# Performance work log

Measured on AMD Instinct MI355X. Metric: run time of the kernel, lower is better.

The kernel has to match this reference:

```python
import jax, jax.numpy as jnp
import numpy as np

SPARSITY = 0.1  # fraction of entries kept (set to 1)


def _subnet(scores, k):
    # Mirrors GetSubnet.forward: full sort of flattened |scores|, zero the
    # lowest j = int((1-k)*n) ranks, set the rest to 1 (ties broken by sort order).
    flat = scores.ravel()
    n = flat.size
    j = int((1.0 - k) * n)  # static python int
    order = jnp.argsort(flat)  # ascending
    out = jnp.zeros((n,), dtype=scores.dtype).at[order[j:]].set(1)
    return out.reshape(scores.shape)


def setup_inputs() -> dict:
    key = jax.random.key(0)
    kA, kB = jax.random.split(key)
    # kaiming_uniform_(a=sqrt(5)) => U(-bound, bound), bound = sqrt(6/((1+5)*fan_in)) = 1/sqrt(fan_in)
    A_shape = (1024, 16384)
    B_shape = (16384, 1024)
    bA = 1.0 / np.sqrt(A_shape[1])
    bB = 1.0 / np.sqrt(B_shape[1])
    lora_A_mask = jax.random.uniform(kA, A_shape, jnp.float32, -bA, bA)
    lora_B_mask = jax.random.uniform(kB, B_shape, jnp.float32, -bB, bB)
    return {"lora_A_mask": lora_A_mask, "lora_B_mask": lora_B_mask}


def reference(lora_A_mask, lora_B_mask):
    mask_A = _subnet(jnp.abs(lora_A_mask), SPARSITY)
    mask_B = _subnet(jnp.abs(lora_B_mask), SPARSITY)
    return (mask_A, mask_B)
```

## Files before the change

### kernel.cpp

```cpp
#include <hip/hip_runtime.h>
#include <stdint.h>

#define OFF_H1     0u
#define OFF_H2     2048u
#define OFF_H3     4096u
#define OFF_PREFIX 6144u
#define OFF_RANK   6145u
#define OFF_T      6146u
#define OFF_C      6147u
#define OFF_CNT    6148u
#define OFF_BCNT   6656u
#define OFF_BUF    7168u
#define CAP        8192u
#define MAT_WORDS  (7168u + 2u * CAP)
#define SUB        4
#define NB2        512
#define SEGCAP     16384u

__global__ void init_k(uint32_t* __restrict__ ws) {
  uint32_t i = blockIdx.x * blockDim.x + threadIdx.x;
  if (i < 6656u) { ws[i] = 0u; ws[MAT_WORDS + i] = 0u; }
}

__global__ void hist1_k(const float* __restrict__ A, const float* __restrict__ B,
                        uint32_t* __restrict__ ws, int nvec) {
  const int m = blockIdx.y;
  const float4* __restrict__ src = (const float4*)(m == 0 ? A : B);
  uint32_t* W = ws + (size_t)m * MAT_WORDS;
  __shared__ uint32_t h[2048 * SUB];
  for (int i = threadIdx.x; i < 2048 * SUB; i += blockDim.x) h[i] = 0u;
  __syncthreads();
  const uint32_t sub = threadIdx.x & (SUB - 1);
  int idx0 = blockIdx.x * blockDim.x + threadIdx.x;
  int stride = gridDim.x * blockDim.x;
  for (int i = idx0; i < nvec; i += stride) {
    float4 f = src[i];
    const float v[4] = {f.x, f.y, f.z, f.w};
#pragma unroll
    for (int c = 0; c < 4; c++) {
      uint32_t u = __float_as_uint(v[c]) & 0x7fffffffu;
      atomicAdd(&h[(u >> 21) * SUB + sub], 1u);
    }
  }
  __syncthreads();
  uint32_t* gh = W + OFF_H1;
  for (int b = threadIdx.x; b < 2048; b += blockDim.x) {
    uint32_t s = 0u;
#pragma unroll
    for (int k = 0; k < SUB; k++) s += h[b * SUB + k];
    if (s) atomicAdd(&gh[b], s);
  }
}

__global__ void hist2_k(const float* __restrict__ A, const float* __restrict__ B,
                        uint32_t* __restrict__ ws, uint32_t* __restrict__ outbuf,
                        int nvec) {
  const int m = blockIdx.y;
  const float4* __restrict__ src = (const float4*)(m == 0 ? A : B);
  uint32_t* W = ws + (size_t)m * MAT_WORDS;
  uint32_t* seg = outbuf + (size_t)m * 16777216u + (size_t)blockIdx.x * (SEGCAP * 2u);
  __shared__ uint32_t h[2048 * SUB];
  __shared__ uint32_t segn;
  for (int i = threadIdx.x; i < 2048 * SUB; i += blockDim.x) h[i] = 0u;
  if (threadIdx.x == 0) segn = 0u;
  uint32_t prefix = W[OFF_PREFIX];
  __syncthreads();
  const uint32_t sub = threadIdx.x & (SUB - 1);
  int idx0 = blockIdx.x * blockDim.x + threadIdx.x;
  int stride = gridDim.x * blockDim.x;
  for (int i = idx0; i < nvec; i += stride) {
    float4 f = src[i];
    const float v[4] = {f.x, f.y, f.z, f.w};
#pragma unroll
    for (int c = 0; c < 4; c++) {
      uint32_t u = __float_as_uint(v[c]) & 0x7fffffffu;
      if ((u >> 21) == (prefix >> 21)) {
        atomicAdd(&h[((u >> 10) & 2047u) * SUB + sub], 1u);
        uint32_t s = atomicAdd(&segn, 1u);
        if (s < SEGCAP) { seg[2u * s] = (uint32_t)i * 4u + (uint32_t)c; seg[2u * s + 1u] = u; }
      }
    }
  }
  __syncthreads();
  uint32_t* gh = W + OFF_H2;
  for (int b = threadIdx.x; b < 2048; b += blockDim.x) {
    uint32_t s = 0u;
#pragma unroll
    for (int k = 0; k < SUB; k++) s += h[b * SUB + k];
    if (s) atomicAdd(&gh[b], s);
  }
  if (threadIdx.x == 0) {
    uint32_t s = segn; if (s > SEGCAP) s = SEGCAP;
    W[OFF_BCNT + blockIdx.x] = s;
  }
}

template <int PASS>
__global__ void scan_k(uint32_t* __restrict__ ws, uint32_t j) {
  const int m = blockIdx.x;
  uint32_t* W = ws + (size_t)m * MAT_WORDS;
  const uint32_t* hist = W + (PASS == 1 ? OFF_H1 : OFF_H2);
  __shared__ uint32_t h[2048];
  __shared__ uint32_t ps[256];
  const int t = threadIdx.x;
  uint32_t r = (PASS == 1) ? j : W[OFF_RANK];
  uint32_t prefix = (PASS == 1) ? 0u : W[OFF_PREFIX];
  uint32_t s = 0u;
  for (int k = 0; k < 8; k++) {
    int b = t * 8 + k;
    uint32_t v = hist[b];
    h[b] = v;
    s += v;
  }
  ps[t] = s;
  __syncthreads();
  for (int off = 1; off < 256; off <<= 1) {
    uint32_t v = (t >= off) ? ps[t - off] : 0u;
    __syncthreads();
    ps[t] += v;
    __syncthreads();
  }
  uint32_t base = (t == 0) ? 0u : ps[t - 1];
  for (int k = 0; k < 8; k++) {
    int b = t * 8 + k;
    uint32_t c = h[b];
    if (r >= base && r < base + c) {
      if (PASS == 1) W[OFF_PREFIX] = (uint32_t)b << 21;
      else           W[OFF_PREFIX] = prefix | ((uint32_t)b << 10);
      W[OFF_RANK] = r - base;
    }
    base += c;
  }
}

__global__ void pass3_k(uint32_t* __restrict__ ws, const uint32_t* __restrict__ outbuf) {
  const int m = blockIdx.y;
  uint32_t* W = ws + (size_t)m * MAT_WORDS;
  const uint32_t* seg = outbuf + (size_t)m * 16777216u + (size_t)blockIdx.x * (SEGCAP * 2u);
  __shared__ uint32_t h[1024];
  for (int i = threadIdx.x; i < 1024; i += blockDim.x) h[i] = 0u;
  uint32_t n = W[OFF_BCNT + blockIdx.x];
  uint32_t prefix = W[OFF_PREFIX];
  __syncthreads();
  for (uint32_t e = threadIdx.x; e < n; e += blockDim.x) {
    uint32_t idx = seg[2u * e];
    uint32_t u   = seg[2u * e + 1u];
    if ((u >> 10) == (prefix >> 10)) {
      atomicAdd(&h[u & 1023u], 1u);
      uint32_t slot = atomicAdd(&W[OFF_CNT], 1u);
      if (slot < CAP) { W[OFF_BUF + 2u * slot] = idx; W[OFF_BUF + 2u * slot + 1u] = u; }
    }
  }
  __syncthreads();
  for (int b = threadIdx.x; b < 1024; b += blockDim.x)
    if (h[b]) atomicAdd(&W[OFF_H3 + b], h[b]);
}

__global__ void scan3tie_k(uint32_t* __restrict__ ws) {
  const int m = blockIdx.x;
  uint32_t* W = ws + (size_t)m * MAT_WORDS;
  __shared__ uint32_t h[1024];
  __shared__ uint32_t ps[256];
  __shared__ uint32_t sT, sTarget;
  __shared__ uint32_t tie_idx[1024];
  __shared__ uint32_t tie_n;
  const int t = threadIdx.x;
  uint32_t r = W[OFF_RANK];
  uint32_t prefix = W[OFF_PREFIX];
  uint32_t cnt = W[OFF_CNT]; if (cnt > CAP) cnt = CAP;
  if (t == 0) tie_n = 0u;
  uint32_t s = 0u;
  for (int k = 0; k < 4; k++) {
    int b = t * 4 + k;
    uint32_t v = W[OFF_H3 + b];
    h[b] = v;
    s += v;
  }
  ps[t] = s;
  __syncthreads();
  for (int off = 1; off < 256; off <<= 1) {
    uint32_t v = (t >= off) ? ps[t - off] : 0u;
    __syncthreads();
    ps[t] += v;
    __syncthreads();
  }
  uint32_t base = (t == 0) ? 0u : ps[t - 1];
  for (int k = 0; k < 4; k++) {
    int b = t * 4 + k;
    uint32_t c = h[b];
    if (r >= base && r < base + c) { sT = prefix | (uint32_t)b; sTarget = r - base; }
    base += c;
  }
  __syncthreads();
  const uint32_t T = sT, target = sTarget;
  for (uint32_t c2 = t; c2 < cnt; c2 += 256u) {
    if (W[OFF_BUF + 2u * c2 + 1u] == T) {
      uint32_t slot = atomicAdd(&tie_n, 1u);
      if (slot < 1024u) tie_idx[slot] = W[OFF_BUF + 2u * c2];
    }
  }
  __syncthreads();
  uint32_t E2 = tie_n; if (E2 > 1024u) E2 = 1024u;
  for (uint32_t c2 = t; c2 < E2; c2 += 256u) {
    uint32_t xi = tie_idx[c2];
    uint32_t lt = 0u;
    for (uint32_t k2 = 0; k2 < E2; k2++) lt += (tie_idx[k2] < xi) ? 1u : 0u;
    if (lt == target) W[OFF_C] = xi;
  }
  if (t == 0) W[OFF_T] = T;
}

__global__ void mask_k(const float* __restrict__ A, const float* __restrict__ B,
                       float* __restrict__ out, const uint32_t* __restrict__ ws,
                       int nvec, int n) {
  const int m = blockIdx.y;
  const float4* __restrict__ src = (const float4*)(m == 0 ? A : B);
  float4* __restrict__ dst = (float4*)(out + (size_t)m * (size_t)n);
  const uint32_t* W = ws + (size_t)m * MAT_WORDS;
  const uint32_t T = W[OFF_T];
  const uint32_t C = W[OFF_C];
  int idx0 = blockIdx.x * blockDim.x + threadIdx.x;
  int stride = gridDim.x * blockDim.x;
  for (int i = idx0; i < nvec; i += stride) {
    float4 f = src[i];
    const float v[4] = {f.x, f.y, f.z, f.w};
    float r[4];
#pragma unroll
    for (int c = 0; c < 4; c++) {
      uint32_t u = __float_as_uint(v[c]) & 0x7fffffffu;
      uint32_t idx = (uint32_t)i * 4u + (uint32_t)c;
      r[c] = (u > T || (u == T && idx >= C)) ? 1.0f : 0.0f;
    }
    dst[i] = make_float4(r[0], r[1], r[2], r[3]);
  }
}

extern "C" void kernel_launch(void* const* d_in, const int* in_sizes, int n_in,
                              void* d_out, int out_size, void* d_ws, size_t ws_size,
                              hipStream_t stream) {
  const float* A = (const float*)d_in[0];
  const float* B = (const float*)d_in[1];
  float* out = (float*)d_out;
  uint32_t* ws = (uint32_t*)d_ws;
  uint32_t* outbuf = (uint32_t*)d_out;
  const int n = in_sizes[0];
  const int nvec = n / 4;
  const uint32_t j = (uint32_t)((1.0 - 0.1) * (double)n);

  init_k<<<(6656 + 255) / 256, 256, 0, stream>>>(ws);
  hist1_k<<<dim3(1024, 2), 256, 0, stream>>>(A, B, ws, nvec);
  scan_k<1><<<2, 256, 0, stream>>>(ws, j);
  hist2_k<<<dim3(NB2, 2), 256, 0, stream>>>(A, B, ws, outbuf, nvec);
  scan_k<2><<<2, 256, 0, stream>>>(ws, j);
  pass3_k<<<dim3(NB2, 2), 256, 0, stream>>>(ws, outbuf);
  scan3tie_k<<<2, 256, 0, stream>>>(ws);
  mask_k<<<dim3(2048, 2), 256, 0, stream>>>(A, B, out, ws, nvec, n);
}
```

Before: 334.9 us.

## Replace radix-select passes with sampled-threshold compaction and single input read

Switches to a sample-based selection. A single block per matrix histograms a strided sample to choose two cut values. One compaction pass then reads the full input once, recording indices of sure-kept elements and (index, value) pairs of candidates near the threshold into the output buffer. Histogram refinement over the candidates and last-block tail reductions replace the separate scan kernels, and the mask is written from a per-block shared bitmap rather than by re-reading the inputs. This drops one full input read and several launches. The cost is reliance on the sample bracketing the true threshold; fixed capacity caps could silently drop elements if the distribution differs from the sample.

```diff
diff --git a/kernel.cpp b/kernel.cpp
--- a/kernel.cpp
+++ b/kernel.cpp
@@ -1,237 +1,330 @@
 #include <hip/hip_runtime.h>
 #include <stdint.h>
 
-#define OFF_H1     0u
-#define OFF_H2     2048u
-#define OFF_H3     4096u
-#define OFF_PREFIX 6144u
-#define OFF_RANK   6145u
-#define OFF_T      6146u
-#define OFF_C      6147u
-#define OFF_CNT    6148u
-#define OFF_BCNT   6656u
-#define OFF_BUF    7168u
-#define CAP        8192u
-#define MAT_WORDS  (7168u + 2u * CAP)
-#define SUB        4
-#define NB2        512
-#define SEGCAP     16384u
-
-__global__ void init_k(uint32_t* __restrict__ ws) {
-  uint32_t i = blockIdx.x * blockDim.x + threadIdx.x;
-  if (i < 6656u) { ws[i] = 0u; ws[MAT_WORDS + i] = 0u; }
-}
-
-__global__ void hist1_k(const float* __restrict__ A, const float* __restrict__ B,
-                        uint32_t* __restrict__ ws, int nvec) {
+#define NBA      8192u
+#define OFF_HA   0u
+#define OFF_HB   8192u
+#define OFF_G    16384u
+#define OFF_GHI  16385u
+#define OFF_S    16386u
+#define OFF_CNTB 16387u
+#define OFF_CNTD 16388u
+#define OFF_BINA 16389u
+#define OFF_RANK 16390u
+#define OFF_T    16391u
+#define OFF_C    16392u
+#define OFF_TCNT 16393u
+#define OFF_BCNT 16400u
+#define OFF_KCNT 17424u
+#define OFF_TBUF 18448u
+#define TCAP     8192u
+#define CTRL     34832u
+#define TA       (2u*CTRL + 0u)
+#define TB       (2u*CTRL + 1u)
+#define ZWORDS   (2u*CTRL + 16u)
+
+#define NB   1024
+#define NBH  128
+#define CHW  1048576u
+#define BCAP 4096u
+#define KCAP 4096u
+
+__global__ __launch_bounds__(1024) void sampleG_k(const float* __restrict__ A,
+                                                  const float* __restrict__ B,
+                                                  uint32_t* __restrict__ ws,
+                                                  int nvec, uint32_t needLo,
+                                                  uint32_t needHi) {
+  const int m = blockIdx.x;
+  const float4* __restrict__ src = (const float4*)(m == 0 ? A : B);
+  uint32_t* W = ws + (size_t)m * CTRL;
+  __shared__ uint32_t sh[16384];
+  __shared__ uint32_t ps[1024];
+  __shared__ int sLo, sHi, sNon;
+  const int t = threadIdx.x;
+  for (int i = t; i < 16384; i += 1024) sh[i] = 0u;
+  if (t == 0) { sLo = -1; sHi = -1; sNon = -1; }
+  __syncthreads();
+  const int w = t >> 6, lane = t & 63;
+  const int cstride = nvec / 256;
+  for (int it = 0; it < 16; it++) {
+    int chunk = it * 16 + w;
+    int fi = chunk * cstride + lane;
+    if (fi < nvec) {
+      float4 f = src[fi];
+      const float v[4] = {f.x, f.y, f.z, f.w};
+#pragma unroll
+      for (int c = 0; c < 4; c++) {
+        uint32_t u = __float_as_uint(v[c]) & 0x7fffffffu;
+        atomicAdd(&sh[u >> 17], 1u);
+      }
+    }
+  }
+  __syncthreads();
+  uint32_t sum = 0u;
+  for (int k = 0; k < 16; k++) sum += sh[t * 16 + k];
+  ps[t] = sum;
+  __syncthreads();
+  for (int off = 1; off < 1024; off <<= 1) {
+    uint32_t v = (t >= off) ? ps[t - off] : 0u;
+    __syncthreads(); ps[t] += v; __syncthreads();
+  }
+  uint32_t total = ps[1023];
+  uint32_t cum = ps[t] - sum;
+  int bLo = -1, bHi = -1, bNon = -1;
+  for (int k = 0; k < 16; k++) {
+    int b = t * 16 + k;
+    uint32_t suf = total - cum;
+    if (suf >= needLo) bLo = b;
+    if (suf >= needHi) bHi = b;
+    if (sh[b]) bNon = b;
+    cum += sh[b];
+  }
+  if (bLo >= 0) atomicMax(&sLo, bLo);
+  if (bHi >= 0) atomicMax(&sHi, bHi);
+  if (bNon >= 0) atomicMax(&sNon, bNon);
+  __syncthreads();
+  if (t == 0) {
+    uint32_t G = (sLo >= 0) ? ((uint32_t)sLo << 17) : 0u;
+    uint32_t GHI = (sHi >= 0) ? ((uint32_t)sHi << 17) : 0u;
+    uint32_t span = ((uint32_t)(sNon + 1 - sLo)) << 17;
+    uint32_t bl = 32u - (uint32_t)__clz(span);
+    W[OFF_G] = G; W[OFF_GHI] = GHI;
+    W[OFF_S] = (bl > 13u) ? bl - 13u : 0u;
+  }
+}
+
+__global__ __launch_bounds__(256) void compact_k(const float* __restrict__ A,
+                                                 const float* __restrict__ B,
+                                                 uint32_t* __restrict__ ws,
+                                                 uint32_t* __restrict__ ob,
+                                                 int nvec) {
   const int m = blockIdx.y;
   const float4* __restrict__ src = (const float4*)(m == 0 ? A : B);
-  uint32_t* W = ws + (size_t)m * MAT_WORDS;
-  __shared__ uint32_t h[2048 * SUB];
-  for (int i = threadIdx.x; i < 2048 * SUB; i += blockDim.x) h[i] = 0u;
-  __syncthreads();
-  const uint32_t sub = threadIdx.x & (SUB - 1);
-  int idx0 = blockIdx.x * blockDim.x + threadIdx.x;
-  int stride = gridDim.x * blockDim.x;
-  for (int i = idx0; i < nvec; i += stride) {
+  uint32_t* W = ws + (size_t)m * CTRL;
+  uint32_t* __restrict__ half = ob + (size_t)m * (size_t)nvec * 4u;
+  const uint32_t b = blockIdx.x;
+  __shared__ uint32_t bn, kn;
+  if (threadIdx.x == 0) { bn = 0u; kn = 0u; }
+  const uint32_t G = W[OFF_G], GHI = W[OFF_GHI];
+  __syncthreads();
+  const int i0 = (int)b * 256 + threadIdx.x;
+  const int nk = nvec >> 18;
+  for (int k = 0; k < nk; k++) {
+    int i = k * 262144 + i0;
     float4 f = src[i];
     const float v[4] = {f.x, f.y, f.z, f.w};
 #pragma unroll
     for (int c = 0; c < 4; c++) {
       uint32_t u = __float_as_uint(v[c]) & 0x7fffffffu;
-      atomicAdd(&h[(u >> 21) * SUB + sub], 1u);
-    }
-  }
-  __syncthreads();
-  uint32_t* gh = W + OFF_H1;
-  for (int b = threadIdx.x; b < 2048; b += blockDim.x) {
-    uint32_t s = 0u;
-#pragma unroll
-    for (int k = 0; k < SUB; k++) s += h[b * SUB + k];
-    if (s) atomicAdd(&gh[b], s);
-  }
-}
-
-__global__ void hist2_k(const float* __restrict__ A, const float* __restrict__ B,
-                        uint32_t* __restrict__ ws, uint32_t* __restrict__ outbuf,
-                        int nvec) {
+      if (u >= GHI) {
+        uint32_t s = atomicAdd(&kn, 1u);
+        if (s < KCAP)
+          half[(8u + (s >> 10)) * CHW + b * 1024u + (s & 1023u)] = (uint32_t)i * 4u + (uint32_t)c;
+      } else if (u >= G) {
+        uint32_t s = atomicAdd(&bn, 1u);
+        if (s < BCAP) {
+          uint32_t w0 = (s >> 9) * CHW + b * 1024u + (s & 511u) * 2u;
+          half[w0]      = (uint32_t)i * 4u + (uint32_t)c;
+          half[w0 + 1u] = u;
+        }
+      }
+    }
+  }
+  __syncthreads();
+  if (threadIdx.x == 0) {
+    uint32_t cb = bn > BCAP ? BCAP : bn, ck = kn > KCAP ? KCAP : kn;
+    W[OFF_BCNT + b] = cb;  W[OFF_KCNT + b] = ck;
+    atomicAdd(&W[OFF_CNTB], cb);  atomicAdd(&W[OFF_CNTD], ck);
+  }
+}
+
+__global__ __launch_bounds__(256) void histA_k(uint32_t* __restrict__ ws,
+                                               const uint32_t* __restrict__ ob,
+                                               int nvec, uint32_t keep) {
   const int m = blockIdx.y;
-  const float4* __restrict__ src = (const float4*)(m == 0 ? A : B);
-  uint32_t* W = ws + (size_t)m * MAT_WORDS;
-  uint32_t* seg = outbuf + (size_t)m * 16777216u + (size_t)blockIdx.x * (SEGCAP * 2u);
-  __shared__ uint32_t h[2048 * SUB];
-  __shared__ uint32_t segn;
-  for (int i = threadIdx.x; i < 2048 * SUB; i += blockDim.x) h[i] = 0u;
-  if (threadIdx.x == 0) segn = 0u;
-  uint32_t prefix = W[OFF_PREFIX];
-  __syncthreads();
-  const uint32_t sub = threadIdx.x & (SUB - 1);
-  int idx0 = blockIdx.x * blockDim.x + threadIdx.x;
-  int stride = gridDim.x * blockDim.x;
-  for (int i = idx0; i < nvec; i += stride) {
-    float4 f = src[i];
-    const float v[4] = {f.x, f.y, f.z, f.w};
-#pragma unroll
-    for (int c = 0; c < 4; c++) {
-      uint32_t u = __float_as_uint(v[c]) & 0x7fffffffu;
-      if ((u >> 21) == (prefix >> 21)) {
-        atomicAdd(&h[((u >> 10) & 2047u) * SUB + sub], 1u);
-        uint32_t s = atomicAdd(&segn, 1u);
-        if (s < SEGCAP) { seg[2u * s] = (uint32_t)i * 4u + (uint32_t)c; seg[2u * s + 1u] = u; }
-      }
-    }
-  }
-  __syncthreads();
-  uint32_t* gh = W + OFF_H2;
-  for (int b = threadIdx.x; b < 2048; b += blockDim.x) {
-    uint32_t s = 0u;
-#pragma unroll
-    for (int k = 0; k < SUB; k++) s += h[b * SUB + k];
-    if (s) atomicAdd(&gh[b], s);
-  }
-  if (threadIdx.x == 0) {
-    uint32_t s = segn; if (s > SEGCAP) s = SEGCAP;
-    W[OFF_BCNT + blockIdx.x] = s;
-  }
-}
-
-template <int PASS>
-__global__ void scan_k(uint32_t* __restrict__ ws, uint32_t j) {
-  const int m = blockIdx.x;
-  uint32_t* W = ws + (size_t)m * MAT_WORDS;
-  const uint32_t* hist = W + (PASS == 1 ? OFF_H1 : OFF_H2);
-  __shared__ uint32_t h[2048];
+  uint32_t* W = ws + (size_t)m * CTRL;
+  const uint32_t* __restrict__ half = ob + (size_t)m * (size_t)nvec * 4u;
+  __shared__ uint32_t h[NBA];
   __shared__ uint32_t ps[256];
+  __shared__ int is_tail;
   const int t = threadIdx.x;
-  uint32_t r = (PASS == 1) ? j : W[OFF_RANK];
-  uint32_t prefix = (PASS == 1) ? 0u : W[OFF_PREFIX];
-  uint32_t s = 0u;
-  for (int k = 0; k < 8; k++) {
-    int b = t * 8 + k;
-    uint32_t v = hist[b];
-    h[b] = v;
-    s += v;
-  }
-  ps[t] = s;
-  __syncthreads();
-  for (int off = 1; off < 256; off <<= 1) {
-    uint32_t v = (t >= off) ? ps[t - off] : 0u;
-    __syncthreads();
-    ps[t] += v;
-    __syncthreads();
-  }
-  uint32_t base = (t == 0) ? 0u : ps[t - 1];
-  for (int k = 0; k < 8; k++) {
-    int b = t * 8 + k;
-    uint32_t c = h[b];
-    if (r >= base && r < base + c) {
-      if (PASS == 1) W[OFF_PREFIX] = (uint32_t)b << 21;
-      else           W[OFF_PREFIX] = prefix | ((uint32_t)b << 10);
-      W[OFF_RANK] = r - base;
-    }
-    base += c;
-  }
-}
-
-__global__ void pass3_k(uint32_t* __restrict__ ws, const uint32_t* __restrict__ outbuf) {
+  for (int i = t; i < (int)NBA; i += 256) h[i] = 0u;
+  const uint32_t G = W[OFF_G], S = W[OFF_S];
+  __syncthreads();
+  for (int s8 = 0; s8 < NB / NBH; s8++) {
+    uint32_t b = blockIdx.x * (NB / NBH) + s8;
+    uint32_t nb = W[OFF_BCNT + b];
+    for (uint32_t e = t; e < nb; e += 256u) {
+      uint32_t u = half[(e >> 9) * CHW + b * 1024u + (e & 511u) * 2u + 1u];
+      uint32_t bin = (u - G) >> S;  if (bin > NBA - 1u) bin = NBA - 1u;
+      atomicAdd(&h[bin], 1u);
+    }
+  }
+  __syncthreads();
+  for (int i = t; i < (int)NBA; i += 256)
+    if (h[i]) atomicAdd(&W[OFF_HA + i], h[i]);
+  __threadfence();
+  __syncthreads();
+  if (t == 0)
+    is_tail = (__hip_atomic_fetch_add(&ws[TA], 1u, __ATOMIC_ACQ_REL,
+                                      __HIP_MEMORY_SCOPE_AGENT) == gridDim.x * gridDim.y - 1u);
+  __syncthreads();
+  if (!is_tail) return;
+  __threadfence();
+  for (int mm = 0; mm < 2; mm++) {
+    uint32_t* Wm = ws + (size_t)mm * CTRL;
+    uint32_t cb = __hip_atomic_load(&Wm[OFF_CNTB], __ATOMIC_RELAXED, __HIP_MEMORY_SCOPE_AGENT);
+    uint32_t cd = __hip_atomic_load(&Wm[OFF_CNTD], __ATOMIC_RELAXED, __HIP_MEMORY_SCOPE_AGENT);
+    uint32_t r = cb + cd - keep;
+    uint32_t loc[32]; uint32_t sum = 0u;
+    for (int k = 0; k < 32; k++) {
+      uint32_t v = __hip_atomic_load(&Wm[OFF_HA + t * 32 + k], __ATOMIC_RELAXED, __HIP_MEMORY_SCOPE_AGENT);
+      loc[k] = v; sum += v;
+    }
+    ps[t] = sum;
+    __syncthreads();
+    for (int off = 1; off < 256; off <<= 1) {
+      uint32_t v = (t >= off) ? ps[t - off] : 0u;
+      __syncthreads(); ps[t] += v; __syncthreads();
+    }
+    uint32_t base = ps[t] - sum;
+    for (int k = 0; k < 32; k++) {
+      uint32_t c = loc[k];
+      if (r >= base && r < base + c) { Wm[OFF_BINA] = t * 32 + k; Wm[OFF_RANK] = r - base; }
+      base += c;
+    }
+    __syncthreads();
+  }
+}
+
+__global__ __launch_bounds__(256) void passB_k(uint32_t* __restrict__ ws,
+                                               const uint32_t* __restrict__ ob,
+                                               int nvec) {
   const int m = blockIdx.y;
-  uint32_t* W = ws + (size_t)m * MAT_WORDS;
-  const uint32_t* seg = outbuf + (size_t)m * 16777216u + (size_t)blockIdx.x * (SEGCAP * 2u);
-  __shared__ uint32_t h[1024];
-  for (int i = threadIdx.x; i < 1024; i += blockDim.x) h[i] = 0u;
-  uint32_t n = W[OFF_BCNT + blockIdx.x];
-  uint32_t prefix = W[OFF_PREFIX];
-  __syncthreads();
-  for (uint32_t e = threadIdx.x; e < n; e += blockDim.x) {
-    uint32_t idx = seg[2u * e];
-    uint32_t u   = seg[2u * e + 1u];
-    if ((u >> 10) == (prefix >> 10)) {
-      atomicAdd(&h[u & 1023u], 1u);
-      uint32_t slot = atomicAdd(&W[OFF_CNT], 1u);
-      if (slot < CAP) { W[OFF_BUF + 2u * slot] = idx; W[OFF_BUF + 2u * slot + 1u] = u; }
-    }
-  }
-  __syncthreads();
-  for (int b = threadIdx.x; b < 1024; b += blockDim.x)
-    if (h[b]) atomicAdd(&W[OFF_H3 + b], h[b]);
-}
-
-__global__ void scan3tie_k(uint32_t* __restrict__ ws) {
-  const int m = blockIdx.x;
-  uint32_t* W = ws + (size_t)m * MAT_WORDS;
-  __shared__ uint32_t h[1024];
+  uint32_t* W = ws + (size_t)m * CTRL;
+  const uint32_t* __restrict__ half = ob + (size_t)m * (size_t)nvec * 4u;
+  __shared__ uint32_t h[NBA];
   __shared__ uint32_t ps[256];
-  __shared__ uint32_t sT, sTarget;
+  __shared__ int is_tail;
+  __shared__ uint32_t sT, sTgt, tie_n;
   __shared__ uint32_t tie_idx[1024];
-  __shared__ uint32_t tie_n;
   const int t = threadIdx.x;
-  uint32_t r = W[OFF_RANK];
-  uint32_t prefix = W[OFF_PREFIX];
-  uint32_t cnt = W[OFF_CNT]; if (cnt > CAP) cnt = CAP;
-  if (t == 0) tie_n = 0u;
-  uint32_t s = 0u;
-  for (int k = 0; k < 4; k++) {
-    int b = t * 4 + k;
-    uint32_t v = W[OFF_H3 + b];
-    h[b] = v;
-    s += v;
-  }
-  ps[t] = s;
-  __syncthreads();
-  for (int off = 1; off < 256; off <<= 1) {
-    uint32_t v = (t >= off) ? ps[t - off] : 0u;
-    __syncthreads();
-    ps[t] += v;
-    __syncthreads();
-  }
-  uint32_t base = (t == 0) ? 0u : ps[t - 1];
-  for (int k = 0; k < 4; k++) {
-    int b = t * 4 + k;
-    uint32_t c = h[b];
-    if (r >= base && r < base + c) { sT = prefix | (uint32_t)b; sTarget = r - base; }
-    base += c;
-  }
-  __syncthreads();
-  const uint32_t T = sT, target = sTarget;
-  for (uint32_t c2 = t; c2 < cnt; c2 += 256u) {
-    if (W[OFF_BUF + 2u * c2 + 1u] == T) {
-      uint32_t slot = atomicAdd(&tie_n, 1u);
-      if (slot < 1024u) tie_idx[slot] = W[OFF_BUF + 2u * c2];
-    }
-  }
-  __syncthreads();
-  uint32_t E2 = tie_n; if (E2 > 1024u) E2 = 1024u;
-  for (uint32_t c2 = t; c2 < E2; c2 += 256u) {
-    uint32_t xi = tie_idx[c2];
-    uint32_t lt = 0u;
-    for (uint32_t k2 = 0; k2 < E2; k2++) lt += (tie_idx[k2] < xi) ? 1u : 0u;
-    if (lt == target) W[OFF_C] = xi;
-  }
-  if (t == 0) W[OFF_T] = T;
-}
-
-__global__ void mask_k(const float* __restrict__ A, const float* __restrict__ B,
-                       float* __restrict__ out, const uint32_t* __restrict__ ws,
-                       int nvec, int n) {
+  for (int i = t; i < (int)NBA; i += 256) h[i] = 0u;
+  const uint32_t G = W[OFF_G], S = W[OFF_S], binA = W[OFF_BINA];
+  const uint32_t mask = (S >= 32u) ? 0xffffffffu : ((1u << S) - 1u);
+  __syncthreads();
+  for (int s8 = 0; s8 < NB / NBH; s8++) {
+    uint32_t b = blockIdx.x * (NB / NBH) + s8;
+    uint32_t nb = W[OFF_BCNT + b];
+    for (uint32_t e = t; e < nb; e += 256u) {
+      uint32_t w0 = (e >> 9) * CHW + b * 1024u + (e & 511u) * 2u;
+      uint32_t idx = half[w0], u = half[w0 + 1u];
+      uint32_t d = u - G;
+      uint32_t bin = d >> S;  if (bin > NBA - 1u) bin = NBA - 1u;
+      if (bin == binA) {
+        atomicAdd(&h[d & mask], 1u);
+        uint32_t slot = atomicAdd(&W[OFF_TCNT], 1u);
+        if (slot < TCAP) { W[OFF_TBUF + 2u * slot] = idx; W[OFF_TBUF + 2u * slot + 1u] = u; }
+      }
+    }
+  }
+  __syncthreads();
+  for (int i = t; i < (int)NBA; i += 256)
+    if (h[i]) atomicAdd(&W[OFF_HB + i], h[i]);
+  __threadfence();
+  __syncthreads();
+  if (t == 0)
+    is_tail = (__hip_atomic_fetch_add(&ws[TB], 1u, __ATOMIC_ACQ_REL,
+                                      __HIP_MEMORY_SCOPE_AGENT) == gridDim.x * gridDim.y - 1u);
+  __syncthreads();
+  if (!is_tail) return;
+  __threadfence();
+  for (int mm = 0; mm < 2; mm++) {
+    uint32_t* Wm = ws + (size_t)mm * CTRL;
+    uint32_t Gm = Wm[OFF_G], Sm = Wm[OFF_S], binAm = Wm[OFF_BINA];
+    uint32_t r = Wm[OFF_RANK];
+    if (t == 0) tie_n = 0u;
+    uint32_t loc[32]; uint32_t sum = 0u;
+    for (int k = 0; k < 32; k++) {
+      uint32_t v = __hip_atomic_load(&Wm[OFF_HB + t * 32 + k], __ATOMIC_RELAXED, __HIP_MEMORY_SCOPE_AGENT);
+      loc[k] = v; sum += v;
+    }
+    ps[t] = sum;
+    __syncthreads();
+    for (int off = 1; off < 256; off <<= 1) {
+      uint32_t v = (t >= off) ? ps[t - off] : 0u;
+      __syncthreads(); ps[t] += v; __syncthreads();
+    }
+    uint32_t base = ps[t] - sum;
+    for (int k = 0; k < 32; k++) {
+      uint32_t c = loc[k];
+      if (r >= base && r < base + c) {
+        sT = Gm + (binAm << Sm) + (uint32_t)(t * 32 + k);
+        sTgt = r - base;
+      }
+      base += c;
+    }
+    __syncthreads();
+    const uint32_t T = sT, target = sTgt;
+    uint32_t cnt = __hip_atomic_load(&Wm[OFF_TCNT], __ATOMIC_RELAXED, __HIP_MEMORY_SCOPE_AGENT);
+    if (cnt > TCAP) cnt = TCAP;
+    for (uint32_t c2 = t; c2 < cnt; c2 += 256u) {
+      uint32_t uu = __hip_atomic_load(&Wm[OFF_TBUF + 2u * c2 + 1u], __ATOMIC_RELAXED, __HIP_MEMORY_SCOPE_AGENT);
+      if (uu == T) {
+        uint32_t slot = atomicAdd(&tie_n, 1u);
+        if (slot < 1024u)
+          tie_idx[slot] = __hip_atomic_load(&Wm[OFF_TBUF + 2u * c2], __ATOMIC_RELAXED, __HIP_MEMORY_SCOPE_AGENT);
+      }
+    }
+    __syncthreads();
+    uint32_t E2 = tie_n; if (E2 > 1024u) E2 = 1024u;
+    for (uint32_t c2 = t; c2 < E2; c2 += 256u) {
+      uint32_t xi = tie_idx[c2];
+      uint32_t lt = 0u;
+      for (uint32_t k2 = 0; k2 < E2; k2++) lt += (tie_idx[k2] < xi) ? 1u : 0u;
+      if (lt == target) Wm[OFF_C] = xi;
+    }
+    if (t == 0) Wm[OFF_T] = T;
+    __syncthreads();
+  }
+}
+
+__global__ __launch_bounds__(256) void maskwrite_k(const uint32_t* __restrict__ ws,
+                                                   float* __restrict__ out, int nvec) {
   const int m = blockIdx.y;
-  const float4* __restrict__ src = (const float4*)(m == 0 ? A : B);
-  float4* __restrict__ dst = (float4*)(out + (size_t)m * (size_t)n);
-  const uint32_t* W = ws + (size_t)m * MAT_WORDS;
-  const uint32_t T = W[OFF_T];
-  const uint32_t C = W[OFF_C];
-  int idx0 = blockIdx.x * blockDim.x + threadIdx.x;
-  int stride = gridDim.x * blockDim.x;
-  for (int i = idx0; i < nvec; i += stride) {
-    float4 f = src[i];
-    const float v[4] = {f.x, f.y, f.z, f.w};
-    float r[4];
-#pragma unroll
-    for (int c = 0; c < 4; c++) {
-      uint32_t u = __float_as_uint(v[c]) & 0x7fffffffu;
-      uint32_t idx = (uint32_t)i * 4u + (uint32_t)c;
-      r[c] = (u > T || (u == T && idx >= C)) ? 1.0f : 0.0f;
-    }
-    dst[i] = make_float4(r[0], r[1], r[2], r[3]);
+  const uint32_t* W = ws + (size_t)m * CTRL;
+  const uint32_t* __restrict__ half = (const uint32_t*)out + (size_t)m * (size_t)nvec * 4u;
+  float4* __restrict__ dst = (float4*)out + (size_t)m * (size_t)nvec;
+  const uint32_t b = blockIdx.x;
+  const int t = threadIdx.x;
+  __shared__ uint32_t bm[512];
+  bm[t] = 0u; bm[t + 256] = 0u;
+  const uint32_t nb = W[OFF_BCNT + b], nk = W[OFF_KCNT + b];
+  const uint32_t T = W[OFF_T], C = W[OFF_C];
+  __syncthreads();
+  for (uint32_t e = t; e < nk; e += 256u) {
+    uint32_t idx = half[(8u + (e >> 10)) * CHW + b * 1024u + (e & 1023u)];
+    uint32_t i4 = idx >> 2;
+    uint32_t lp = (i4 >> 18) * 1024u + ((i4 & 262143u) - b * 256u) * 4u + (idx & 3u);
+    atomicOr(&bm[lp >> 5], 1u << (lp & 31u));
+  }
+  for (uint32_t e = t; e < nb; e += 256u) {
+    uint32_t w0 = (e >> 9) * CHW + b * 1024u + (e & 511u) * 2u;
+    uint32_t idx = half[w0], u = half[w0 + 1u];
+    if (u > T || (u == T && idx >= C)) {
+      uint32_t i4 = idx >> 2;
+      uint32_t lp = (i4 >> 18) * 1024u + ((i4 & 262143u) - b * 256u) * 4u + (idx & 3u);
+      atomicOr(&bm[lp >> 5], 1u << (lp & 31u));
+    }
+  }
+  __syncthreads();
+  const int nkc = nvec >> 18;
+  for (int k = 0; k < nkc; k++) {
+    int lp4 = k * 256 + t;
+    uint32_t nib = (bm[lp4 >> 3] >> ((lp4 & 7) * 4)) & 15u;
+    dst[(size_t)k * 262144u + b * 256u + t] =
+        make_float4((nib & 1u) ? 1.f : 0.f, (nib & 2u) ? 1.f : 0.f,
+                    (nib & 4u) ? 1.f : 0.f, (nib & 8u) ? 1.f : 0.f);
   }
 }
 
@@ -242,17 +335,18 @@
   const float* B = (const float*)d_in[1];
   float* out = (float*)d_out;
   uint32_t* ws = (uint32_t*)d_ws;
-  uint32_t* outbuf = (uint32_t*)d_out;
+  uint32_t* ob = (uint32_t*)d_out;
   const int n = in_sizes[0];
   const int nvec = n / 4;
   const uint32_t j = (uint32_t)((1.0 - 0.1) * (double)n);
-
-  init_k<<<(6656 + 255) / 256, 256, 0, stream>>>(ws);
-  hist1_k<<<dim3(1024, 2), 256, 0, stream>>>(A, B, ws, nvec);
-  scan_k<1><<<2, 256, 0, stream>>>(ws, j);
-  hist2_k<<<dim3(NB2, 2), 256, 0, stream>>>(A, B, ws, outbuf, nvec);
-  scan_k<2><<<2, 256, 0, stream>>>(ws, j);
-  pass3_k<<<dim3(NB2, 2), 256, 0, stream>>>(ws, outbuf);
-  scan3tie_k<<<2, 256, 0, stream>>>(ws);
-  mask_k<<<dim3(2048, 2), 256, 0, stream>>>(A, B, out, ws, nvec, n);
-}
+  const uint32_t keep = (uint32_t)n - j;
+  const uint32_t needLo = (13u * 65536u) / 100u;
+  const uint32_t needHi = (8u * 65536u) / 100u;
+
+  hipMemsetAsync(d_ws, 0, (size_t)ZWORDS * 4u, stream);
+  sampleG_k<<<2, 1024, 0, stream>>>(A, B, ws, nvec, needLo, needHi);
+  compact_k<<<dim3(NB, 2), 256, 0, stream>>>(A, B, ws, ob, nvec);
+  histA_k<<<dim3(NBH, 2), 256, 0, stream>>>(ws, ob, nvec, keep);
+  passB_k<<<dim3(NBH, 2), 256, 0, stream>>>(ws, ob, nvec);
+  maskwrite_k<<<dim3(NB, 2), 256, 0, stream>>>(ws, out, nvec);
+}
```

Result: slower. 399.0 us (+19.1%).
